# Performance work log

Measured on AMD Instinct MI355X. Metric: run time of the kernel, lower is better.

Reference implementation:

```python
import jax, jax.numpy as jnp
import numpy as np
from jax import lax

# SLAYER neuron / simulation constants (netParams)
THETA = 1.0      # spike threshold
TAU_SR = 4.0     # PSP (SRM) kernel time constant
TAU_REF = 1.0    # refractory kernel time constant
SCALE_REF = 2.0  # refractory scale (kernel amplitude = -scaleRef*theta)
TAU_RHO = 1.0    # surrogate-gradient width (used in bwd only)
SCALE_RHO = 1.0

B, F_IN, T = 8, 6300, 500  # 6300 = 50*63*2
HID, OUT = 32, 20


def _alpha_scan(x, d):
    """Causal conv with alpha kernel k*d**k along last (time) axis via 2-state recurrence.
    x: [..., T]. y[t] = sum_{j<=t} x[j]*(t-j)*d**(t-j)."""
    xt = jnp.moveaxis(x, -1, 0)  # [T, ...]
    zero = jnp.zeros_like(xt[0])

    def step(carry, xi):
        z, y = carry
        y_new = d * (y + z)       # y[t] = d*(y[t-1] + z[t-1])
        z_new = d * z + xi        # z[t] = d*z[t-1] + x[t]
        return (z_new, y_new), y_new

    _, ys = lax.scan(step, (zero, zero), xt)
    return jnp.moveaxis(ys, 0, -1)


def psp(x):
    """SLAYER psp: convolve spike train with SRM kernel eps(k) = (k/tauSr)*exp(1-k/tauSr)."""
    d = float(np.exp(-1.0 / TAU_SR))
    return jnp.float32(np.e / TAU_SR) * _alpha_scan(x, d)


def _spike_impl(p):
    """Iterative threshold + refractory. p: [..., T] membrane input (post-psp, post-dense).
    Refractory kernel: ref(k) = -scaleRef*theta*(k/tauRef)*exp(1-k/tauRef), realized by the
    same 2-state alpha recurrence driven by emitted spikes."""
    d = float(np.exp(-1.0 / TAU_REF))
    C = jnp.float32(-SCALE_REF * THETA * np.e / TAU_REF)
    pt = jnp.moveaxis(p, -1, 0)  # [T, ...]
    zero = jnp.zeros_like(pt[0])

    def step(carry, pi):
        z, y = carry
        y_new = d * (y + z)                 # alpha state from past spikes (lag>=1)
        u = pi + C * y_new                  # membrane potential incl. refractory
        s = (u >= THETA).astype(pi.dtype)   # hard threshold
        z_new = d * z + s
        return (z_new, y_new), s

    _, ss = lax.scan(step, (zero, zero), pt)
    return jnp.moveaxis(ss, 0, -1)


def spike(p):
    return _spike_impl(p)


def setup_inputs() -> dict:
    key = jax.random.key(0)
    k1, k2, k3 = jax.random.split(key, 3)
    downsampled = (jax.random.uniform(k1, (B, F_IN, T)) < 0.05).astype(jnp.float32)
    w1 = jax.random.normal(k2, (HID, F_IN), jnp.float32) * 0.05
    w2 = jax.random.normal(k3, (OUT, HID), jnp.float32) * 0.3
    return {"downsampled": downsampled, "w1": w1, "w2": w2}


def reference(downsampled, w1, w2):
    # spike_1 = spike(psp(downsampled))
    s1 = spike(psp(downsampled))
    # spike_2 = spike(fc1(psp(spike_1)))
    s2 = spike(jnp.einsum('of,bft->bot', w1, psp(s1)))
    # spike_3 = spike(fc2(psp(spike_2)))
    s3 = spike(jnp.einsum('of,bft->bot', w2, psp(s2)))
    return s3
```

## Files before the change

### kernel.cpp

```cpp
#include <hip/hip_runtime.h>
#include <stdint.h>

#define NB 8
#define F_IN 6300
#define NT 500
#define HID 32
#define NOUT 20
#define NW 99

#define D_SR   0.7788007830714049f
#define S_SR   0.6795704571147613f
#define D_REF  0.36787944117144233f
#define C_REF  -5.43656365691809f

__global__ __launch_bounds__(256) void k0_transpose(const float* __restrict__ w1,
                                                    float* __restrict__ w1t) {
  __shared__ float tl[64][33];
  const int f0 = blockIdx.x * 64;
  const int tid = threadIdx.x;
  const int r = tid & 63, g = tid >> 6;
#pragma unroll
  for (int oo = 0; oo < 32; oo += 4) {
    int o = oo + g;
    int f = f0 + r;
    tl[r][o] = (f < F_IN) ? w1[o * F_IN + f] : 0.f;
  }
  __syncthreads();
#pragma unroll
  for (int k = 0; k < 8; k++) {
    int idx = k * 256 + tid;
    int rr = idx >> 5, cc = idx & 31;
    int f = f0 + rr;
    if (f < F_IN) w1t[(size_t)f * 32 + cc] = tl[rr][cc];
  }
}

#define CH_T 100

__global__ __launch_bounds__(64, 1) void k1_layer1(const float* __restrict__ x,
                                                   uint64_t* __restrict__ masks) {
  __shared__ __align__(16) float tileT[64][104];
  const int wi = blockIdx.x;
  const int b  = blockIdx.y;
  const int lane = threadIdx.x;
  const int f = wi * 64 + lane;
  const uint64_t vmask = __ballot(f < F_IN);
  const float* xblk = x + (size_t)b * F_IN * NT;
  uint64_t* mrow = masks + ((size_t)b * NW + wi) * NT;

  int goff[25], doff[25];
#pragma unroll
  for (int k = 0; k < 25; k++) {
    int idx = k * 64 + lane;
    int fid = idx / 25;
    int j = idx - fid * 25;
    int rf = wi * 64 + fid;
    if (rf >= F_IN) rf = F_IN - 1;
    goff[k] = rf * NT + 4 * j;
    doff[k] = fid * 104 + 4 * j;
  }

  float z1 = 0.f, y1 = 0.f, zr = 0.f, yr = 0.f;
  float* tbase = &tileT[0][0];

#pragma unroll 1
  for (int c = 0; c < 5; c++) {
    const float* gb = xblk + c * CH_T;
    float4 ld[25];
#pragma unroll
    for (int k = 0; k < 25; k++) ld[k] = *(const float4*)(gb + goff[k]);
#pragma unroll
    for (int k = 0; k < 25; k++) *(float4*)(tbase + doff[k]) = ld[k];

    const float4* lrow = (const float4*)&tileT[lane][0];
    float4 rbuf[4];
#pragma unroll
    for (int i = 0; i < 4; i++) rbuf[i] = lrow[i];
    uint64_t keep0 = 0, keep1 = 0;
#pragma unroll
    for (int g = 0; g < 25; g++) {
      float4 xq = rbuf[g & 3];
      if (g + 4 < 25) rbuf[g & 3] = lrow[g + 4];
      float xs[4] = {xq.x, xq.y, xq.z, xq.w};
#pragma unroll
      for (int e = 0; e < 4; e++) {
        const int tc = g * 4 + e;
        float xi = xs[e];
        y1 = __fmul_rn(D_SR, __fadd_rn(y1, z1));
        z1 = __fadd_rn(__fmul_rn(D_SR, z1), xi);
        float p = __fmul_rn(S_SR, y1);
        yr = __fmul_rn(D_REF, __fadd_rn(yr, zr));
        float u = __fadd_rn(p, __fmul_rn(C_REF, yr));
        bool s = (u >= 1.0f);
        zr = __fadd_rn(__fmul_rn(D_REF, zr), s ? 1.0f : 0.0f);
        uint64_t m = __ballot(s);
        if (tc < 64) { if (lane == tc)      keep0 = m; }
        else         { if (lane == tc - 64) keep1 = m; }
      }
    }
    uint64_t* mp = mrow + c * CH_T;
    mp[lane] = keep0 & vmask;
    if (lane < CH_T - 64) mp[64 + lane] = keep1 & vmask;
  }
}

__global__ __launch_bounds__(512) void k2_fc1(const float* __restrict__ w1t,
                                              const uint64_t* __restrict__ masks,
                                              double* __restrict__ R) {
  __shared__ double part[8][32];
  const int tid = threadIdx.x;
  const int wv = tid >> 6;
  const int lane = tid & 63;
  const int half = lane >> 5;
  const int o = lane & 31;
  const int b = blockIdx.x;
  const int t = blockIdx.y * 4 + (wv & 3);
  const int seg = wv >> 2;
  const int wbeg = seg * 50, wend = seg ? NW : 50;
  const uint64_t* mbase = masks + (size_t)b * NW * NT + t;
  const char* wrow = (const char*)w1t + o * 4;
  double acc0 = 0.0, acc1 = 0.0, acc2 = 0.0, acc3 = 0.0;

  int wi = wbeg + half;
  uint64_t mcur = (wi < wend) ? mbase[(size_t)wi * NT] : 0;
  for (; wi < wend; wi += 2) {
    uint64_t mnext = (wi + 2 < wend) ? mbase[(size_t)(wi + 2) * NT] : 0;
    const uint32_t base0 = ((uint32_t)wi << 13);
    uint32_t w = (uint32_t)mcur;
    uint32_t boff = base0;
#pragma unroll
    for (int sub = 0; sub < 2; sub++) {
      while (w) {
        uint32_t i0 = __builtin_ctz(w);                 uint32_t w1_ = w & (w - 1);
        uint32_t i1 = w1_ ? __builtin_ctz(w1_) : 0u;    uint32_t w2_ = w1_ ? (w1_ & (w1_ - 1)) : 0u;
        uint32_t i2 = w2_ ? __builtin_ctz(w2_) : 0u;    uint32_t w3_ = w2_ ? (w2_ & (w2_ - 1)) : 0u;
        uint32_t i3 = w3_ ? __builtin_ctz(w3_) : 0u;    w = w3_ ? (w3_ & (w3_ - 1)) : 0u;
        float a0 = *(const float*)(wrow + boff + (i0 << 7));
        float a1 = *(const float*)(wrow + boff + (i1 << 7));
        float a2 = *(const float*)(wrow + boff + (i2 << 7));
        float a3 = *(const float*)(wrow + boff + (i3 << 7));
        a1 = w1_ ? a1 : 0.0f;
        a2 = w2_ ? a2 : 0.0f;
        a3 = w3_ ? a3 : 0.0f;
        acc0 += (double)a0;
        acc1 += (double)a1;
        acc2 += (double)a2;
        acc3 += (double)a3;
      }
      w = (uint32_t)(mcur >> 32);
      boff = base0 + (32u << 7);
    }
    mcur = mnext;
  }
  double acc = (acc0 + acc1) + (acc2 + acc3);
  int hi2 = __shfl_xor(__double2hiint(acc), 32);
  int lo2 = __shfl_xor(__double2loint(acc), 32);
  acc += __hiloint2double(hi2, lo2);
  if (half == 0) part[wv][o] = acc;
  __syncthreads();
  if (wv < 4 && half == 0) {
    double tot = part[wv][o] + part[wv + 4][o];
    R[((size_t)b * HID + o) * NT + t] = tot;
  }
}

#define SNN_FAST_STEP(rin, EMIT)                                                \
  {                                                                             \
    y2 = __builtin_fma(dsr, y2, w);                                   \
    z2 = __builtin_fma(dsr, z2, (rin));                               \
    w  = dsr * z2;                                                              \
    double p  = ssr * y2;                                                       \
    double u0 = __builtin_fma(cr, q, p);                                        \
    double u1 = u0 + K;                                                         \
    double u  = sp ? u1 : u0;                                                   \
    bool s = (u >= 1.0);                                                        \
    double yr = q + (sp ? dre : 0.0);                                 \
    double zr = zrd + (sp ? 1.0 : 0.0);                           \
    zrd = dre * zr;                                                             \
    q = __builtin_fma(dre, yr, dre * zrd);                             \
    sp = s;                                                                     \
    EMIT                                                                        \
  }

__global__ __launch_bounds__(64) void k3_spike2(const double* __restrict__ R,
                                                uint32_t* __restrict__ s2m) {
  const int blk = blockIdx.x;
  const int lane = threadIdx.x;
  const int half = lane >> 5;
  const int b = blk * 2 + half;
  const int h = lane & 31;
  const double2* r2 = (const double2*)(R + ((size_t)b * HID + h) * NT);
  uint32_t* m0 = s2m + (size_t)(blk * 2) * NT;
  uint32_t* m1 = s2m + (size_t)(blk * 2 + 1) * NT;

  const double dsr = (double)D_SR, ssr = (double)S_SR;
  const double dre = (double)D_REF, cr = (double)C_REF;
  const double K = cr * dre;
  double y2 = 0, z2 = 0, w = 0, q = 0, zrd = 0;
  bool sp = false;

  double2 bufa[8], bufb[8];
#pragma unroll
  for (int i = 0; i < 8; i++) { bufa[i] = r2[i * 2]; bufb[i] = r2[i * 2 + 1]; }

  for (int g8 = 0; g8 < 16; g8++) {
#pragma unroll
    for (int j = 0; j < 8; j++) {
      const int g = g8 * 8 + j;
      if (g >= 125) break;
      const int t = g * 4;
      double2 va = bufa[j], vb = bufb[j];
      SNN_FAST_STEP(va.x, { uint64_t m = __ballot(s);
        if (lane == 0) { m0[t] = (uint32_t)m; m1[t] = (uint32_t)(m >> 32); } })
      SNN_FAST_STEP(va.y, { uint64_t m = __ballot(s);
        if (lane == 0) { m0[t + 1] = (uint32_t)m; m1[t + 1] = (uint32_t)(m >> 32); } })
      SNN_FAST_STEP(vb.x, { uint64_t m = __ballot(s);
        if (lane == 0) { m0[t + 2] = (uint32_t)m; m1[t + 2] = (uint32_t)(m >> 32); } })
      SNN_FAST_STEP(vb.y, { uint64_t m = __ballot(s);
        if (lane == 0) { m0[t + 3] = (uint32_t)m; m1[t + 3] = (uint32_t)(m >> 32); } })
      if (g + 8 < 125) { bufa[j] = r2[(g + 8) * 2]; bufb[j] = r2[(g + 8) * 2 + 1]; }
    }
  }
}

__global__ __launch_bounds__(256) void k4_fc2(const float* __restrict__ w2,
                                              const uint32_t* __restrict__ s2m,
                                              double* __restrict__ R3) {
  __shared__ float w2l[NOUT * HID];
  const int tid = threadIdx.x;
  for (int i = tid; i < NOUT * HID; i += 256) w2l[i] = w2[i];
  __syncthreads();
  int id = blockIdx.x * 256 + tid;
  if (id >= NB * NOUT * NT) return;
  int t = id % NT;
  int bo = id / NT;
  int o = bo % NOUT;
  int b = bo / NOUT;
  uint32_t m = s2m[(size_t)b * NT + t];
  const float* wr = w2l + o * HID;
  double acc = 0.0;
  while (m) {
    uint32_t i0 = __builtin_ctz(m);                 uint32_t m1_ = m & (m - 1);
    uint32_t i1 = m1_ ? __builtin_ctz(m1_) : 0u;    uint32_t m2_ = m1_ ? (m1_ & (m1_ - 1)) : 0u;
    uint32_t i2 = m2_ ? __builtin_ctz(m2_) : 0u;    uint32_t m3_ = m2_ ? (m2_ & (m2_ - 1)) : 0u;
    uint32_t i3 = m3_ ? __builtin_ctz(m3_) : 0u;    m = m3_ ? (m3_ & (m3_ - 1)) : 0u;
    float a0 = wr[i0];
    float a1 = m1_ ? wr[i1] : 0.0f;
    float a2 = m2_ ? wr[i2] : 0.0f;
    float a3 = m3_ ? wr[i3] : 0.0f;
    acc += (double)a0;
    acc += (double)a1;
    acc += (double)a2;
    acc += (double)a3;
  }
  R3[id] = acc;
}

__global__ __launch_bounds__(64) void k5_out(const double* __restrict__ R3,
                                             float* __restrict__ out) {
  int id = blockIdx.x * 64 + threadIdx.x;
  if (id >= NB * NOUT) return;
  const double2* r2 = (const double2*)(R3 + (size_t)id * NT);
  float* orow = out + (size_t)id * NT;

  const double dsr = (double)D_SR, ssr = (double)S_SR;
  const double dre = (double)D_REF, cr = (double)C_REF;
  const double K = cr * dre;
  double y2 = 0, z2 = 0, w = 0, q = 0, zrd = 0;
  bool sp = false;

  double2 bufa[8], bufb[8];
#pragma unroll
  for (int i = 0; i < 8; i++) { bufa[i] = r2[i * 2]; bufb[i] = r2[i * 2 + 1]; }

  for (int g8 = 0; g8 < 16; g8++) {
#pragma unroll
    for (int j = 0; j < 8; j++) {
      const int g = g8 * 8 + j;
      if (g >= 125) break;
      double2 va = bufa[j], vb = bufb[j];
      float4 ov;
      SNN_FAST_STEP(va.x, { ov.x = s ? 1.0f : 0.0f; })
      SNN_FAST_STEP(va.y, { ov.y = s ? 1.0f : 0.0f; })
      SNN_FAST_STEP(vb.x, { ov.z = s ? 1.0f : 0.0f; })
      SNN_FAST_STEP(vb.y, { ov.w = s ? 1.0f : 0.0f; })
      *(float4*)(orow + g * 4) = ov;
      if (g + 8 < 125) { bufa[j] = r2[(g + 8) * 2]; bufb[j] = r2[(g + 8) * 2 + 1]; }
    }
  }
}

extern "C" void kernel_launch(void* const* d_in, const int* in_sizes, int n_in,
                              void* d_out, int out_size, void* d_ws, size_t ws_size,
                              hipStream_t stream) {
  const float* x  = (const float*)d_in[0];
  const float* w1 = (const float*)d_in[1];
  const float* w2 = (const float*)d_in[2];
  float* out = (float*)d_out;

  uint8_t* ws = (uint8_t*)d_ws;
  const size_t W1T_BYTES  = (size_t)F_IN * HID * 4;
  const size_t MASK_BYTES = (size_t)NB * NW * NT * 8;
  const size_t R_BYTES    = (size_t)NB * HID * NT * 8;
  const size_t S2M_BYTES  = (size_t)NB * NT * 4;
  float*    w1t   = (float*)ws;
  uint64_t* masks = (uint64_t*)(ws + W1T_BYTES);
  double*   R     = (double*)(ws + W1T_BYTES + MASK_BYTES);
  uint32_t* s2m   = (uint32_t*)(ws + W1T_BYTES + MASK_BYTES + R_BYTES);
  double*   R3    = (double*)(ws + W1T_BYTES + MASK_BYTES + R_BYTES + S2M_BYTES);

  k0_transpose<<<99, 256, 0, stream>>>(w1, w1t);
  k1_layer1<<<dim3(NW, NB), 64, 0, stream>>>(x, masks);
  k2_fc1<<<dim3(NB, NT / 4), 512, 0, stream>>>(w1t, masks, R);
  k3_spike2<<<4, 64, 0, stream>>>(R, s2m);
  k4_fc2<<<(NB * NOUT * NT + 255) / 256, 256, 0, stream>>>(w2, s2m, R3);
  k5_out<<<3, 64, 0, stream>>>(R3, out);
}
```

Baseline: 281.1 us.

## Fuse fc2 into output spike kernel, widen fc1 blocks, unpad layer1 tile

Merges the fc2 mask-dot kernel into the final spiking kernel, so each output thread computes its own fc2 input on the fly from layer-2 spike masks and the R3 round trip and one launch go away. Doubles the fc1 block to 1024 threads, splitting the feature windows into four segments instead of two to add parallelism per block. Also shrinks the layer-1 shared tile row pitch from 104 to 100 floats. The fused kernel puts fc2 work onto the serial per-neuron recurrence in only 3 blocks, and the tighter tile pitch may add LDS bank conflicts.

```diff
diff --git a/kernel.cpp b/kernel.cpp
--- a/kernel.cpp
+++ b/kernel.cpp
@@ -39,7 +39,7 @@
 
 __global__ __launch_bounds__(64, 1) void k1_layer1(const float* __restrict__ x,
                                                    uint64_t* __restrict__ masks) {
-  __shared__ __align__(16) float tileT[64][104];
+  __shared__ __align__(16) float tileT[64][100];
   const int wi = blockIdx.x;
   const int b  = blockIdx.y;
   const int lane = threadIdx.x;
@@ -57,7 +57,7 @@
     int rf = wi * 64 + fid;
     if (rf >= F_IN) rf = F_IN - 1;
     goff[k] = rf * NT + 4 * j;
-    doff[k] = fid * 104 + 4 * j;
+    doff[k] = fid * 100 + 4 * j;
   }
 
   float z1 = 0.f, y1 = 0.f, zr = 0.f, yr = 0.f;
@@ -104,10 +104,10 @@
   }
 }
 
-__global__ __launch_bounds__(512) void k2_fc1(const float* __restrict__ w1t,
-                                              const uint64_t* __restrict__ masks,
-                                              double* __restrict__ R) {
-  __shared__ double part[8][32];
+__global__ __launch_bounds__(1024) void k2_fc1(const float* __restrict__ w1t,
+                                               const uint64_t* __restrict__ masks,
+                                               double* __restrict__ R) {
+  __shared__ double part[16][32];
   const int tid = threadIdx.x;
   const int wv = tid >> 6;
   const int lane = tid & 63;
@@ -116,7 +116,8 @@
   const int b = blockIdx.x;
   const int t = blockIdx.y * 4 + (wv & 3);
   const int seg = wv >> 2;
-  const int wbeg = seg * 50, wend = seg ? NW : 50;
+  const int wbeg = seg * 25;
+  const int wend = (seg == 3) ? NW : (wbeg + 25);
   const uint64_t* mbase = masks + (size_t)b * NW * NT + t;
   const char* wrow = (const char*)w1t + o * 4;
   double acc0 = 0.0, acc1 = 0.0, acc2 = 0.0, acc3 = 0.0;
@@ -159,8 +160,8 @@
   if (half == 0) part[wv][o] = acc;
   __syncthreads();
   if (wv < 4 && half == 0) {
-    double tot = part[wv][o] + part[wv + 4][o];
-    R[((size_t)b * HID + o) * NT + t] = tot;
+    double tot = ((part[wv][o] + part[wv + 4][o]) + part[wv + 8][o]) + part[wv + 12][o];
+    R[((size_t)b * HID + o) * NT + (blockIdx.y * 4 + wv)] = tot;
   }
 }
 
@@ -223,21 +224,7 @@
   }
 }
 
-__global__ __launch_bounds__(256) void k4_fc2(const float* __restrict__ w2,
-                                              const uint32_t* __restrict__ s2m,
-                                              double* __restrict__ R3) {
-  __shared__ float w2l[NOUT * HID];
-  const int tid = threadIdx.x;
-  for (int i = tid; i < NOUT * HID; i += 256) w2l[i] = w2[i];
-  __syncthreads();
-  int id = blockIdx.x * 256 + tid;
-  if (id >= NB * NOUT * NT) return;
-  int t = id % NT;
-  int bo = id / NT;
-  int o = bo % NOUT;
-  int b = bo / NOUT;
-  uint32_t m = s2m[(size_t)b * NT + t];
-  const float* wr = w2l + o * HID;
+__device__ __forceinline__ double mask_dot(uint32_t m, const float* __restrict__ wr) {
   double acc = 0.0;
   while (m) {
     uint32_t i0 = __builtin_ctz(m);                 uint32_t m1_ = m & (m - 1);
@@ -253,14 +240,22 @@
     acc += (double)a2;
     acc += (double)a3;
   }
-  R3[id] = acc;
-}
-
-__global__ __launch_bounds__(64) void k5_out(const double* __restrict__ R3,
-                                             float* __restrict__ out) {
-  int id = blockIdx.x * 64 + threadIdx.x;
+  return acc;
+}
+
+__global__ __launch_bounds__(64) void k45_out(const float* __restrict__ w2,
+                                              const uint32_t* __restrict__ s2m,
+                                              float* __restrict__ out) {
+  __shared__ float w2l[NOUT][33];
+  const int tid = threadIdx.x;
+  for (int i = tid; i < NOUT * HID; i += 64) w2l[i >> 5][i & 31] = w2[i];
+  __syncthreads();
+  int id = blockIdx.x * 64 + tid;
   if (id >= NB * NOUT) return;
-  const double2* r2 = (const double2*)(R3 + (size_t)id * NT);
+  int b = id / NOUT;
+  int o = id - b * NOUT;
+  const uint4* m4 = (const uint4*)(s2m + (size_t)b * NT);
+  const float* wr = &w2l[o][0];
   float* orow = out + (size_t)id * NT;
 
   const double dsr = (double)D_SR, ssr = (double)S_SR;
@@ -269,23 +264,27 @@
   double y2 = 0, z2 = 0, w = 0, q = 0, zrd = 0;
   bool sp = false;
 
-  double2 bufa[8], bufb[8];
-#pragma unroll
-  for (int i = 0; i < 8; i++) { bufa[i] = r2[i * 2]; bufb[i] = r2[i * 2 + 1]; }
-
-  for (int g8 = 0; g8 < 16; g8++) {
-#pragma unroll
-    for (int j = 0; j < 8; j++) {
-      const int g = g8 * 8 + j;
+  uint4 mbuf[4];
+#pragma unroll
+  for (int i = 0; i < 4; i++) mbuf[i] = m4[i];
+
+  for (int g4 = 0; g4 < 32; g4++) {
+#pragma unroll
+    for (int j = 0; j < 4; j++) {
+      const int g = g4 * 4 + j;
       if (g >= 125) break;
-      double2 va = bufa[j], vb = bufb[j];
+      uint4 mq = mbuf[j];
+      if (g + 4 < 125) mbuf[j] = m4[g + 4];
+      double r0 = mask_dot(mq.x, wr);
+      double r1 = mask_dot(mq.y, wr);
+      double r2v = mask_dot(mq.z, wr);
+      double r3v = mask_dot(mq.w, wr);
       float4 ov;
-      SNN_FAST_STEP(va.x, { ov.x = s ? 1.0f : 0.0f; })
-      SNN_FAST_STEP(va.y, { ov.y = s ? 1.0f : 0.0f; })
-      SNN_FAST_STEP(vb.x, { ov.z = s ? 1.0f : 0.0f; })
-      SNN_FAST_STEP(vb.y, { ov.w = s ? 1.0f : 0.0f; })
+      SNN_FAST_STEP(r0,  { ov.x = s ? 1.0f : 0.0f; })
+      SNN_FAST_STEP(r1,  { ov.y = s ? 1.0f : 0.0f; })
+      SNN_FAST_STEP(r2v, { ov.z = s ? 1.0f : 0.0f; })
+      SNN_FAST_STEP(r3v, { ov.w = s ? 1.0f : 0.0f; })
       *(float4*)(orow + g * 4) = ov;
-      if (g + 8 < 125) { bufa[j] = r2[(g + 8) * 2]; bufb[j] = r2[(g + 8) * 2 + 1]; }
     }
   }
 }
@@ -302,17 +301,14 @@
   const size_t W1T_BYTES  = (size_t)F_IN * HID * 4;
   const size_t MASK_BYTES = (size_t)NB * NW * NT * 8;
   const size_t R_BYTES    = (size_t)NB * HID * NT * 8;
-  const size_t S2M_BYTES  = (size_t)NB * NT * 4;
   float*    w1t   = (float*)ws;
   uint64_t* masks = (uint64_t*)(ws + W1T_BYTES);
   double*   R     = (double*)(ws + W1T_BYTES + MASK_BYTES);
   uint32_t* s2m   = (uint32_t*)(ws + W1T_BYTES + MASK_BYTES + R_BYTES);
-  double*   R3    = (double*)(ws + W1T_BYTES + MASK_BYTES + R_BYTES + S2M_BYTES);
 
   k0_transpose<<<99, 256, 0, stream>>>(w1, w1t);
   k1_layer1<<<dim3(NW, NB), 64, 0, stream>>>(x, masks);
-  k2_fc1<<<dim3(NB, NT / 4), 512, 0, stream>>>(w1t, masks, R);
+  k2_fc1<<<dim3(NB, NT / 4), 1024, 0, stream>>>(w1t, masks, R);
   k3_spike2<<<4, 64, 0, stream>>>(R, s2m);
-  k4_fc2<<<(NB * NOUT * NT + 255) / 256, 256, 0, stream>>>(w2, s2m, R3);
-  k5_out<<<3, 64, 0, stream>>>(R3, out);
-}
+  k45_out<<<3, 64, 0, stream>>>(w2, s2m, out);
+}
```

After: 539.3 us. +91.8%, slower.
